# Kernel optimization log

Hardware: AMD Instinct MI355X
Metric: run time of the kernel (lower is better)

Reference implementation:

```python
import jax, jax.numpy as jnp
import numpy as np

B, C_IN, N, K, UP = 4, 128, 1024, 9, 4
EPS_BN = 1e-5


def _grid():
    # gen_grid(4): num_x=num_y=2, linspace(-0.2,0.2,2) -> (4,2)
    g = jnp.linspace(-0.2, 0.2, 2)
    x, y = jnp.meshgrid(g, g, indexing='ij')
    return jnp.stack([x, y], axis=-1).reshape(-1, 2)


def _knn(x, k, dilation):
    # x: (B,C,N). L2-normalize features, matrix pairwise dist, top-k, dilated select.
    nrm = jnp.sqrt(jnp.sum(x * x, axis=1, keepdims=True))
    xn = x / jnp.maximum(nrm, 1e-12)
    xt = xn.transpose(0, 2, 1)                      # (B,N,C)
    sq = jnp.sum(xt * xt, axis=-1)                  # (B,N)
    dist = sq[:, :, None] - 2.0 * jnp.einsum('bnc,bmc->bnm', xt, xt) + sq[:, None, :]
    _, idx = jax.lax.top_k(-dist, k * dilation)     # k*d nearest (incl. self)
    return idx[:, :, ::dilation]                    # (B,N,k)


def _bn(x, g, b, axes):
    # training-mode batchnorm over given axes, channel axis = 1
    m = jnp.mean(x, axis=axes, keepdims=True)
    v = jnp.mean((x - m) ** 2, axis=axes, keepdims=True)
    sh = [1] * x.ndim
    sh[1] = -1
    return (x - m) * jax.lax.rsqrt(v + EPS_BN) * g.reshape(sh) + b.reshape(sh)


def _edge_conv(x, k, dil, W, g, b):
    # DGCNN edge conv: gather neighbors, [x_i, x_j-x_i], 1x1 conv, BN, relu, max over k
    idx = _knn(x, k, dil)                                        # (B,N,k)
    x_j = jax.vmap(lambda xx, ii: xx[:, ii])(x, idx)             # (B,C,N,k)
    x_i = jnp.broadcast_to(x[..., None], x_j.shape)
    feat = jnp.concatenate([x_i, x_j - x_i], axis=1)             # (B,2C,N,k)
    out = jnp.einsum('oc,bcnk->bonk', W, feat)
    out = jax.nn.relu(_bn(out, g, b, (0, 2, 3)))
    return jnp.max(out, axis=-1)                                 # (B,Cout,N)


def _conv1d(x, W, b):
    return jnp.einsum('oc,bcn->bon', W, x) + b[None, :, None]


def _atten(x, Wf, bf, gf, bef, Wg, bg, gg, beg, Wh, bh, gh, beh, gamma):
    # attention_unit / RA_Layer1 math (C=130)
    f = jax.nn.relu(_bn(_conv1d(x, Wf, bf), gf, bef, (0, 2)))    # (B,C/4,M)
    g_ = jax.nn.relu(_bn(_conv1d(x, Wg, bg), gg, beg, (0, 2)))
    h = jax.nn.relu(_bn(_conv1d(x, Wh, bh), gh, beh, (0, 2)))    # (B,C,M)
    s = jnp.einsum('bcn,bcm->bnm', g_, f)                        # g^T @ f: (B,M,M)
    beta = jax.nn.softmax(s, axis=2)
    o = jnp.einsum('bcn,bnm->bcm', h, beta)                      # h @ beta
    return gamma * o + x


def _forward(inp, Wa, gna, bta, Wb, gnb, btb, Wf, bf, gf, bef, Wg, bg, gg, beg,
             Wh, bh, gh, beh, gamma, W1, b1, W2, b2):
    x1 = _edge_conv(inp, K, 1, Wa, gna, bta)                     # (B,256,N)
    x2 = _edge_conv(inp, K, 2, Wb, gnb, btb)                     # (B,256,N)
    x = jnp.concatenate([x1, x2], axis=1)                        # (B,512,N)
    net = x.transpose(0, 2, 1).reshape(B, N * UP, 128)           # (B,4N,128)
    grid = jnp.repeat(_grid(), N, axis=0)                        # (4N,2)
    grid = jnp.broadcast_to(grid[None], (B, N * UP, 2)).astype(net.dtype)
    net = jnp.concatenate([net, grid], axis=2).transpose(0, 2, 1)  # (B,130,4N)
    net = _atten(net, Wf, bf, gf, bef, Wg, bg, gg, beg, Wh, bh, gh, beh, gamma)
    net = jax.nn.relu(_conv1d(net, W1, b1))                      # 130->256
    net = jax.nn.relu(_conv1d(net, W2, b2))                      # 256->128
    return net                                                   # (B,128,4N)


def setup_inputs() -> dict:
    key = jax.random.key(0)
    ks = jax.random.split(key, 24)
    rn = lambda k, sh, s=0.05: jax.random.normal(k, sh, jnp.float32) * s
    d = {
        'inp': jax.random.normal(ks[0], (B, C_IN, N), jnp.float32),
        'Wa': rn(ks[1], (256, 256)), 'gna': 1.0 + rn(ks[2], (256,)), 'bta': rn(ks[3], (256,)),
        'Wb': rn(ks[4], (256, 256)), 'gnb': 1.0 + rn(ks[5], (256,)), 'btb': rn(ks[6], (256,)),
        'Wf': rn(ks[7], (32, 130)), 'bf': rn(ks[8], (32,)), 'gf': 1.0 + rn(ks[9], (32,)), 'bef': rn(ks[9], (32,)),
        'Wg': rn(ks[10], (32, 130)), 'bg': rn(ks[11], (32,)), 'gg': 1.0 + rn(ks[12], (32,)), 'beg': rn(ks[12], (32,)),
        'Wh': rn(ks[13], (130, 130)), 'bh': rn(ks[14], (130,)), 'gh': 1.0 + rn(ks[15], (130,)), 'beh': rn(ks[15], (130,)),
        'gamma': rn(ks[16], (), 1.0),
        'W1': rn(ks[17], (256, 130)), 'b1': rn(ks[18], (256,)),
        'W2': rn(ks[19], (128, 256)), 'b2': rn(ks[20], (128,)),
    }
    return d


def reference(inp, Wa, gna, bta, Wb, gnb, btb, Wf, bf, gf, bef, Wg, bg, gg, beg,
              Wh, bh, gh, beh, gamma, W1, b1, W2, b2):
    return _forward(inp, Wa, gna, bta, Wb, gnb, btb, Wf, bf, gf, bef, Wg, bg, gg, beg,
                    Wh, bh, gh, beh, gamma, W1, b1, W2, b2)
```

## Files before the change

### kernel.cpp

```cpp
#include <hip/hip_runtime.h>

namespace {
constexpr int NB = 4;
constexpr int CI = 128;
constexpr int NP = 1024;
constexpr int MM = 4096;
constexpr float EPSBN = 1e-5f;
constexpr float LOG2E = 1.4426950408889634f;

constexpr size_t OPS_SH = 2162688;
constexpr size_t OFF_OP   = 0;
constexpr size_t OFF_DIST = 0;
constexpr size_t OFF_PM   = 0;
constexpr size_t OFF_QM   = 2097152;
constexpr size_t OFF_HRAW = 0;
constexpr size_t OFF_FGRAW= 2359296;
constexpr size_t OFF_Y1   = 0;
constexpr size_t OFF_FGT  = 6488064;
constexpr size_t OFF_HB   = 7012352;
constexpr size_t OFF_A16  = 6488064;
constexpr size_t OFF_X16  = 8192000;
constexpr size_t OFF_LSE  = 9502720;
constexpr size_t OFF_LSEP = 9519104;
constexpr size_t OFF_STATS= 9650176;
constexpr size_t OFF_ABE  = 9715712;
constexpr size_t OFF_ABFG = 9716736;
constexpr size_t OFF_ABH  = 9716864;
constexpr size_t OFF_FGP  = 9717376;
constexpr size_t OFF_BIAS = 9725568;
constexpr size_t OFF_W16  = 9726208;
constexpr size_t OFF_KNN  = 9779712;
constexpr size_t OFF_XN   = 9853440;
constexpr size_t OFF_SQ   = 10377728;
constexpr size_t OFF_XR   = 10381824;
constexpr size_t OFF_WPQ  = 10643968;
constexpr size_t W16_FG = 0;
constexpr size_t W16_H  = 10240;
constexpr size_t W16_C1 = 33280;
constexpr size_t W16_C2 = 74240;
constexpr size_t B_FG = 0, B_H = 64, B_C1 = 208, B_C2 = 464;
}

typedef __attribute__((ext_vector_type(8))) short short8;
typedef __attribute__((ext_vector_type(4))) float f32x4;
#define MFMA16(A, B, C) __builtin_amdgcn_mfma_f32_16x16x32_bf16(A, B, C, 0, 0, 0)

__device__ inline unsigned short f2bf(float x) {
  unsigned int u = __float_as_uint(x);
  unsigned int r = u + 0x7fff + ((u >> 16) & 1);
  return (unsigned short)(r >> 16);
}
__device__ inline float bf2f(unsigned short s) {
  return __uint_as_float(((unsigned int)s) << 16);
}
__device__ inline unsigned cvtpk(float lo, float hi) {
  unsigned r;
  asm("v_cvt_pk_bf16_f32 %0, %1, %2" : "=v"(r) : "v"(lo), "v"(hi));
  return r;
}

__global__ __launch_bounds__(256) void k_prep(const float* __restrict__ Wf, const float* __restrict__ Wg,
                                              const float* __restrict__ Wh, const float* __restrict__ W1,
                                              const float* __restrict__ W2, const float* __restrict__ bf,
                                              const float* __restrict__ bg, const float* __restrict__ bh,
                                              const float* __restrict__ b1, const float* __restrict__ b2,
                                              const float* __restrict__ Wa, const float* __restrict__ Wb,
                                              unsigned short* __restrict__ W16, float* __restrict__ BIAS,
                                              unsigned short* __restrict__ WPQ) {
  int i = blockIdx.x * 256 + threadIdx.x;
  if (i < 107008) {
    float v = 0.f;
    if (i < 10240) { int o = i / 160, c = i % 160; if (c < 130) v = (o < 32) ? Wf[o * 130 + c] : Wg[(o - 32) * 130 + c]; }
    else if (i < 33280) { int r = i - 10240; int o = r / 160, c = r % 160; if (o < 130 && c < 130) v = Wh[o * 130 + c]; }
    else if (i < 74240) { int r = i - 33280; int o = r / 160, c = r % 160; if (c < 130) v = W1[o * 130 + c]; }
    else { int r = i - 74240; int o = r / 256, c = r % 256; v = W2[o * 256 + c]; }
    W16[i] = f2bf(v);
  } else if (i < 107648) {
    int j = i - 107008; float v = 0.f;
    if (j < 64) v = (j < 32) ? bf[j] : bg[j - 32];
    else if (j < 208) { int c = j - 64; if (c < 130) v = bh[c]; }
    else if (j < 464) v = b1[j - 208];
    else if (j < 592) v = b2[j - 464];
    BIAS[j] = v;
  } else if (i < 238720) {
    int j = i - 107648;
    int e = j >> 16;
    int rem = j & 65535;
    int pq = rem >> 15;
    int rr = rem & 32767;
    int o = rr >> 7, c = rr & 127;
    const float* W = e ? Wb : Wa;
    float w1 = W[o * 256 + c], w2 = W[o * 256 + 128 + c];
    float v = pq ? w2 : (w1 - w2);
    WPQ[j] = f2bf(v);
  }
}

__global__ __launch_bounds__(256) void k_norm(const float* __restrict__ x,
                                              float* __restrict__ xn,
                                              unsigned short* __restrict__ XR,
                                              float* __restrict__ sq) {
  int t = blockIdx.x * 256 + threadIdx.x;
  int b = t >> 10, n = t & 1023;
  const float* xb = x + (size_t)b * CI * NP + n;
  float ss = 0.f;
  #pragma unroll 4
  for (int c = 0; c < CI; ++c) { float v = xb[(size_t)c * NP]; ss += v * v; }
  float inv = 1.f / fmaxf(sqrtf(ss), 1e-12f);
  float* xo = xn + (size_t)b * CI * NP + n;
  float s2 = 0.f;
  for (int c0 = 0; c0 < 128; c0 += 8) {
    unsigned rw[4];
    #pragma unroll
    for (int j = 0; j < 4; ++j) {
      float va = xb[(size_t)(c0 + 2 * j) * NP];
      float vb = xb[(size_t)(c0 + 2 * j + 1) * NP];
      float na = va * inv, nb = vb * inv;
      s2 += na * na + nb * nb;
      xo[(size_t)(c0 + 2 * j) * NP] = na;
      xo[(size_t)(c0 + 2 * j + 1) * NP] = nb;
      rw[j] = (unsigned)f2bf(va) | ((unsigned)f2bf(vb) << 16);
    }
    uint4 r4 = {rw[0], rw[1], rw[2], rw[3]};
    *(uint4*)&XR[(size_t)t * 128 + c0] = r4;
  }
  sq[t] = s2;
}

__global__ __launch_bounds__(256) void k_dist(const float* __restrict__ xn,
                                              const float* __restrict__ sq,
                                              float* __restrict__ dist) {
  __shared__ float As[32][132], Bs[32][132];
  int t = threadIdx.x;
  int m0 = blockIdx.x * 128, n0 = blockIdx.y * 128, b = blockIdx.z;
  int mg = t & 15, ng = t >> 4;
  float acc[8][8];
  #pragma unroll
  for (int i = 0; i < 8; ++i)
    #pragma unroll
    for (int j = 0; j < 8; ++j) acc[i][j] = 0.f;
  for (int cc = 0; cc < 128; cc += 32) {
    __syncthreads();
    for (int idx = t; idx < 4096; idx += 256) {
      int c = idx >> 7, j = idx & 127;
      As[c][j] = xn[((size_t)b * CI + cc + c) * NP + n0 + j];
      Bs[c][j] = xn[((size_t)b * CI + cc + c) * NP + m0 + j];
    }
    __syncthreads();
    #pragma unroll
    for (int c = 0; c < 32; ++c) {
      float4 a0 = *(const float4*)&As[c][ng * 8];
      float4 a1 = *(const float4*)&As[c][ng * 8 + 4];
      float4 b0 = *(const float4*)&Bs[c][mg * 8];
      float4 b1 = *(const float4*)&Bs[c][mg * 8 + 4];
      float av[8] = {a0.x, a0.y, a0.z, a0.w, a1.x, a1.y, a1.z, a1.w};
      float bv[8] = {b0.x, b0.y, b0.z, b0.w, b1.x, b1.y, b1.z, b1.w};
      #pragma unroll
      for (int i = 0; i < 8; ++i)
        #pragma unroll
        for (int j = 0; j < 8; ++j) acc[i][j] += av[i] * bv[j];
    }
  }
  #pragma unroll
  for (int i = 0; i < 8; ++i) {
    int n = n0 + ng * 8 + i;
    float sn = sq[b * NP + n];
    #pragma unroll
    for (int jq = 0; jq < 2; ++jq) {
      float4 r;
      int mb = m0 + mg * 8 + jq * 4;
      r.x = sn + sq[b * NP + mb + 0] - 2.f * acc[i][jq * 4 + 0];
      r.y = sn + sq[b * NP + mb + 1] - 2.f * acc[i][jq * 4 + 1];
      r.z = sn + sq[b * NP + mb + 2] - 2.f * acc[i][jq * 4 + 2];
      r.w = sn + sq[b * NP + mb + 3] - 2.f * acc[i][jq * 4 + 3];
      *(float4*)&dist[((size_t)b * NP + n) * NP + mb] = r;
    }
  }
}

__global__ __launch_bounds__(64) void k_knn(const float* __restrict__ dist,
                                            int* __restrict__ knn) {
  int row = blockIdx.x;
  int l = threadIdx.x;
  const float* dr = dist + (size_t)row * NP;
  float d[16];
  #pragma unroll
  for (int i = 0; i < 16; ++i) d[i] = dr[l + 64 * i];
  for (int s = 0; s < 18; ++s) {
    float best = __builtin_inff(); int bslot = -1;
    #pragma unroll
    for (int i = 0; i < 16; ++i) if (d[i] < best) { best = d[i]; bslot = i; }
    int bidx = (bslot >= 0) ? (l + 64 * bslot) : 0x7fffffff;
    float bd = best; int bi = bidx;
    #pragma unroll
    for (int off = 32; off > 0; off >>= 1) {
      float od = __shfl_xor(bd, off);
      int   oi = __shfl_xor(bi, off);
      if (od < bd || (od == bd && oi < bi)) { bd = od; bi = oi; }
    }
    if (l == 0) knn[row * 18 + s] = bi;
    if ((bi & 63) == l) d[bi >> 6] = __builtin_inff();
  }
}

__global__ __launch_bounds__(256) void k_pqm(const unsigned short* __restrict__ XR,
                                             const unsigned short* __restrict__ WPQ,
                                             float* __restrict__ Pm,
                                             float* __restrict__ Qm) {
  int t = threadIdx.x; int w = t >> 6; int l = t & 63;
  int lm = l & 15, g = l >> 4;
  int nt = blockIdx.x, oq = blockIdx.y, z = blockIdx.z;
  int e = z >> 2, b = z & 3;
  int srow = nt * 64 + w * 16 + lm;
  const unsigned short* sp = XR + ((size_t)b * 1024 + srow) * 128 + 8 * g;
  const unsigned short* wpp = WPQ + ((size_t)(e * 2 + 0) * 256 + oq * 64 + lm) * 128 + 8 * g;
  const unsigned short* wqq = WPQ + ((size_t)(e * 2 + 1) * 256 + oq * 64 + lm) * 128 + 8 * g;
  f32x4 accp[4], accq[4];
  #pragma unroll
  for (int i = 0; i < 4; ++i) { accp[i] = {0.f, 0.f, 0.f, 0.f}; accq[i] = {0.f, 0.f, 0.f, 0.f}; }
  #pragma unroll
  for (int cc = 0; cc < 4; ++cc) {
    short8 bfr = *(const short8*)(sp + cc * 32);
    #pragma unroll
    for (int ct = 0; ct < 4; ++ct) {
      short8 ap = *(const short8*)(wpp + (size_t)ct * 16 * 128 + cc * 32);
      accp[ct] = MFMA16(ap, bfr, accp[ct]);
      short8 aq = *(const short8*)(wqq + (size_t)ct * 16 * 128 + cc * 32);
      accq[ct] = MFMA16(aq, bfr, accq[ct]);
    }
  }
  int eb = e * 4 + b;
  #pragma unroll
  for (int ct = 0; ct < 4; ++ct) {
    int o0 = oq * 64 + ct * 16 + 4 * g;
    float4 rp = {accp[ct][0], accp[ct][1], accp[ct][2], accp[ct][3]};
    float4 rq = {accq[ct][0], accq[ct][1], accq[ct][2], accq[ct][3]};
    *(float4*)&Pm[((size_t)eb * 1024 + srow) * 256 + o0] = rp;
    *(float4*)&Qm[((size_t)eb * 1024 + srow) * 256 + o0] = rq;
  }
}

__global__ __launch_bounds__(256) void k_edge_stats(const float* __restrict__ Pm,
                                                    const float* __restrict__ Qm,
                                                    const int* __restrict__ knn,
                                                    float* __restrict__ stats) {
  int o = threadIdx.x;
  int chunk = blockIdx.x, b = blockIdx.y, e = blockIdx.z;
  int eb = e * 4 + b;
  float s = 0.f, s2 = 0.f;
  for (int nn = 0; nn < 64; ++nn) {
    int n = chunk * 64 + nn;
    float p = Pm[((size_t)eb * 1024 + n) * 256 + o];
    const int* kn = knn + (b * 1024 + n) * 18;
    #pragma unroll
    for (int kk = 0; kk < 9; ++kk) {
      int j = kn[e ? 2 * kk : kk];
      float v = p + Qm[((size_t)eb * 1024 + j) * 256 + o];
      s += v; s2 += v * v;
    }
  }
  size_t idx = ((((size_t)e * 4 + b) * 16 + chunk) * 256 + o) * 2;
  stats[idx] = s; stats[idx + 1] = s2;
}

__global__ __launch_bounds__(256) void k_edge_fin(const float* __restrict__ stats,
                                                  const float* __restrict__ gna, const float* __restrict__ bta,
                                                  const float* __restrict__ gnb, const float* __restrict__ btb,
                                                  float* __restrict__ ab) {
  int i = blockIdx.x * 256 + threadIdx.x;
  if (i >= 512) return;
  int e = i >> 8, o = i & 255;
  float s = 0.f, s2 = 0.f;
  for (int b = 0; b < 4; ++b)
    for (int ch = 0; ch < 16; ++ch) {
      size_t idx = ((((size_t)e * 4 + b) * 16 + ch) * 256 + o) * 2;
      s += stats[idx]; s2 += stats[idx + 1];
    }
  float cnt = 4.0f * 1024.0f * 9.0f;
  float mean = s / cnt;
  float var = s2 / cnt - mean * mean;
  float g = e ? gnb[o] : gna[o];
  float bt = e ? btb[o] : bta[o];
  float alpha = g * rsqrtf(var + EPSBN);
  ab[i * 2] = alpha; ab[i * 2 + 1] = bt - mean * alpha;
}

__global__ __launch_bounds__(256) void k_edge_apply(const float* __restrict__ Pm,
                                                    const float* __restrict__ Qm,
                                                    const int* __restrict__ knn,
                                                    const float* __restrict__ ab,
                                                    unsigned short* __restrict__ X16) {
  __shared__ int knl[18];
  int t = threadIdx.x;
  int n = blockIdx.x, b = blockIdx.y;
  if (t < 18) knl[t] = knn[(b * 1024 + n) * 18 + t];
  __syncthreads();
  int e = t >> 7, oo = t & 127;
  int eb = e * 4 + b;
  const float* Pr = Pm + ((size_t)eb * 1024 + n) * 256;
  const float* Qb = Qm + (size_t)eb * 1024 * 256;
  float p0 = Pr[oo], p1 = Pr[oo + 128];
  float a0 = ab[(e * 256 + oo) * 2], be0 = ab[(e * 256 + oo) * 2 + 1];
  float a1 = ab[(e * 256 + oo + 128) * 2], be1 = ab[(e * 256 + oo + 128) * 2 + 1];
  float mx0 = -__builtin_inff(), mx1 = -__builtin_inff();
  #pragma unroll
  for (int kk = 0; kk < 9; ++kk) {
    int j = knl[e ? 2 * kk : kk];
    const float* Qr = Qb + (size_t)j * 256;
    mx0 = fmaxf(mx0, fmaf(a0, p0 + Qr[oo], be0));
    mx1 = fmaxf(mx1, fmaf(a1, p1 + Qr[oo + 128], be1));
  }
  int u0 = e << 1, u1 = (e << 1) | 1;
  X16[((size_t)b * MM + 4 * n + u0) * 160 + oo] = f2bf(fmaxf(mx0, 0.f));
  X16[((size_t)b * MM + 4 * n + u1) * 160 + oo] = f2bf(fmaxf(mx1, 0.f));
  if (t < 128) {
    int u = t >> 5, c = 128 + (t & 31);
    int gr = n >> 8;
    float v = (c == 128) ? ((gr < 2) ? -0.2f : 0.2f) : (c == 129) ? ((gr & 1) ? 0.2f : -0.2f) : 0.f;
    X16[((size_t)b * MM + 4 * n + u) * 160 + c] = f2bf(v);
  }
}

template <int KSTEPS, int CTPER, int OUTMODE, bool RELU>
__global__ __launch_bounds__(256) void k_convm(const unsigned short* __restrict__ src,
                                               const unsigned short* __restrict__ W16,
                                               const float* __restrict__ bias,
                                               float* __restrict__ dstF,
                                               unsigned short* __restrict__ dstB,
                                               int outld, int rows) {
  constexpr int LD = KSTEPS * 32;
  int t = threadIdx.x; int w = t >> 6; int l = t & 63;
  int lm = l & 15, g = l >> 4;
  int b = blockIdx.z; int ct0 = blockIdx.y * CTPER;
  int srow = blockIdx.x * 64 + w * 16 + lm;
  const unsigned short* sp = src + ((size_t)b * MM + srow) * LD + 8 * g;
  const unsigned short* wp = W16 + ((size_t)ct0 * 16 + lm) * LD + 8 * g;
  f32x4 acc[CTPER];
  #pragma unroll
  for (int i = 0; i < CTPER; ++i) acc[i] = {0.f, 0.f, 0.f, 0.f};
  #pragma unroll
  for (int cc = 0; cc < KSTEPS; ++cc) {
    short8 bfr = *(const short8*)(sp + cc * 32);
    #pragma unroll
    for (int ct = 0; ct < CTPER; ++ct) {
      short8 af = *(const short8*)(wp + (size_t)ct * 16 * LD + cc * 32);
      acc[ct] = MFMA16(af, bfr, acc[ct]);
    }
  }
  #pragma unroll
  for (int ct = 0; ct < CTPER; ++ct) {
    int o0 = (ct0 + ct) * 16 + 4 * g;
    float4 bv = *(const float4*)&bias[o0];
    float v[4] = {acc[ct][0] + bv.x, acc[ct][1] + bv.y, acc[ct][2] + bv.z, acc[ct][3] + bv.w};
    if (RELU) { v[0] = fmaxf(v[0], 0.f); v[1] = fmaxf(v[1], 0.f); v[2] = fmaxf(v[2], 0.f); v[3] = fmaxf(v[3], 0.f); }
    if (OUTMODE == 0) {
      float4 r = {v[0], v[1], v[2], v[3]};
      *(float4*)&dstF[((size_t)b * MM + srow) * outld + o0] = r;
    } else if (OUTMODE == 1) {
      uint2 pk;
      pk.x = cvtpk(v[0], v[1]);
      pk.y = cvtpk(v[2], v[3]);
      *(uint2*)&dstB[((size_t)b * MM + srow) * outld + o0] = pk;
    } else {
      #pragma unroll
      for (int r = 0; r < 4; ++r)
        dstF[((size_t)b * rows + o0 + r) * MM + srow] = v[r];
    }
  }
}

__global__ __launch_bounds__(256) void k_fgstats(const float* __restrict__ FGraw,
                                                 float* __restrict__ FGP) {
  __shared__ float red[4][64][2];
  int t = threadIdx.x; int c = t & 63, rq = t >> 6;
  int blk = blockIdx.x;
  float s = 0.f, s2 = 0.f;
  for (int k = 0; k < 64; ++k) {
    int r = blk * 256 + rq + 4 * k;
    float v = FGraw[(size_t)r * 64 + c];
    s += v; s2 += v * v;
  }
  red[rq][c][0] = s; red[rq][c][1] = s2;
  __syncthreads();
  if (t < 64) {
    float a = 0.f, a2 = 0.f;
    #pragma unroll
    for (int q = 0; q < 4; ++q) { a += red[q][t][0]; a2 += red[q][t][1]; }
    FGP[((size_t)blk * 64 + t) * 2] = a; FGP[((size_t)blk * 64 + t) * 2 + 1] = a2;
  }
}

__global__ __launch_bounds__(64) void k_fgfin(const float* __restrict__ FGP,
                                              const float* __restrict__ gf, const float* __restrict__ bef,
                                              const float* __restrict__ gg, const float* __restrict__ beg,
                                              float* __restrict__ ab) {
  int c = threadIdx.x;
  float s = 0.f, s2 = 0.f;
  for (int blk = 0; blk < 64; ++blk) { s += FGP[((size_t)blk * 64 + c) * 2]; s2 += FGP[((size_t)blk * 64 + c) * 2 + 1]; }
  float cnt = 16384.f;
  float mean = s / cnt, var = s2 / cnt - mean * mean;
  float gv = (c < 32) ? gf[c] : gg[c - 32];
  float bv = (c < 32) ? bef[c] : beg[c - 32];
  float alpha = gv * rsqrtf(var + EPSBN);
  ab[c * 2] = alpha; ab[c * 2 + 1] = bv - mean * alpha;
}

__global__ __launch_bounds__(256) void k_bnstats(const float* __restrict__ src,
                                                 const float* __restrict__ g,
                                                 const float* __restrict__ be,
                                                 float* __restrict__ ab, int ldC) {
  int o = blockIdx.x;
  int t = threadIdx.x;
  float s = 0.f, s2 = 0.f;
  for (int b = 0; b < NB; ++b) {
    const float* r = src + ((size_t)b * ldC + o) * MM;
    for (int m = t; m < MM; m += 256) { float v = r[m]; s += v; s2 += v * v; }
  }
  __shared__ float rs[256], rs2[256];
  rs[t] = s; rs2[t] = s2;
  __syncthreads();
  for (int off = 128; off > 0; off >>= 1) {
    if (t < off) { rs[t] += rs[t + off]; rs2[t] += rs2[t + off]; }
    __syncthreads();
  }
  if (t == 0) {
    float cnt = 16384.0f;
    float mean = rs[0] / cnt, var = rs2[0] / cnt - mean * mean;
    float alpha = g[o] * rsqrtf(var + EPSBN);
    ab[o * 2] = alpha; ab[o * 2 + 1] = be[o] - mean * alpha;
  }
}

__global__ __launch_bounds__(256) void k_cvtFG(const float* __restrict__ FGraw,
                                               const float* __restrict__ ab,
                                               unsigned short* __restrict__ FGT) {
  int i = blockIdx.x * 256 + threadIdx.x;
  int row = i >> 3, c0 = (i & 7) * 8;
  float sc = (c0 < 32) ? LOG2E : 1.0f;
  float vv[8];
  float4 u0 = *(const float4*)&FGraw[(size_t)row * 64 + c0];
  float4 u1 = *(const float4*)&FGraw[(size_t)row * 64 + c0 + 4];
  vv[0] = u0.x; vv[1] = u0.y; vv[2] = u0.z; vv[3] = u0.w;
  vv[4] = u1.x; vv[5] = u1.y; vv[6] = u1.z; vv[7] = u1.w;
  uint4 pk;
  unsigned pw[4];
  #pragma unroll
  for (int h = 0; h < 4; ++h) {
    int c = c0 + 2 * h;
    float a0 = ab[c * 2] * sc, b0 = ab[c * 2 + 1] * sc;
    float a1 = ab[(c + 1) * 2] * sc, b1 = ab[(c + 1) * 2 + 1] * sc;
    float x0 = fmaxf(fmaf(a0, vv[2 * h], b0), 0.f);
    float x1 = fmaxf(fmaf(a1, vv[2 * h + 1], b1), 0.f);
    pw[h] = cvtpk(x0, x1);
  }
  pk.x = pw[0]; pk.y = pw[1]; pk.z = pw[2]; pk.w = pw[3];
  *(uint4*)&FGT[(size_t)row * 64 + c0] = pk;
}

__global__ __launch_bounds__(256) void k_cvtH(const float* __restrict__ src,
                                              const float* __restrict__ ab,
                                              unsigned short* __restrict__ dst) {
  int i = blockIdx.x * 256 + threadIdx.x;
  int m4 = i & 1023; int c = (i >> 10) % 144; int b = i / (144 * 1024);
  ushort4 ov = {0, 0, 0, 0};
  if (c < 130) {
    float4 v = *(const float4*)&src[((size_t)b * 144 + c) * MM + m4 * 4];
    float a = ab[c * 2], be = ab[c * 2 + 1];
    ov.x = f2bf(fmaxf(fmaf(a, v.x, be), 0.f));
    ov.y = f2bf(fmaxf(fmaf(a, v.y, be), 0.f));
    ov.z = f2bf(fmaxf(fmaf(a, v.z, be), 0.f));
    ov.w = f2bf(fmaxf(fmaf(a, v.w, be), 0.f));
  }
  *(ushort4*)&dst[((size_t)b * 144 + c) * MM + m4 * 4] = ov;
}

__global__ __launch_bounds__(256) void k_zlse(const unsigned short* __restrict__ FGT,
                                              float* __restrict__ LSEP) {
  int t = threadIdx.x; int w = t >> 6; int l = t & 63;
  int b = blockIdx.z; int ms = blockIdx.y;
  int n0 = blockIdx.x * 64 + w * 16;
  int lm = l & 15, g = l >> 4;
  f32x4 z4 = {0.f, 0.f, 0.f, 0.f};
  short8 af = *(const short8*)&FGT[((size_t)b * MM + n0 + lm) * 64 + 32 + 8 * g];
  float rm[4], zz[4];
  #pragma unroll
  for (int r = 0; r < 4; ++r) { rm[r] = -__builtin_inff(); zz[r] = 0.f; }
  for (int it = 0; it < 16; ++it) {
    int m0 = ms * 1024 + it * 64;
    short8 bfr[4];
    #pragma unroll
    for (int mi = 0; mi < 4; ++mi)
      bfr[mi] = *(const short8*)&FGT[((size_t)b * MM + m0 + mi * 16 + lm) * 64 + 8 * g];
    f32x4 d[4];
    #pragma unroll
    for (int mi = 0; mi < 4; ++mi) d[mi] = MFMA16(af, bfr[mi], z4);
    #pragma unroll
    for (int r = 0; r < 4; ++r) {
      float tm = fmaxf(fmaxf(d[0][r], d[1][r]), fmaxf(d[2][r], d[3][r]));
      float nm = fmaxf(rm[r], tm);
      zz[r] = zz[r] * exp2f(rm[r] - nm)
            + exp2f(d[0][r] - nm) + exp2f(d[1][r] - nm)
            + exp2f(d[2][r] - nm) + exp2f(d[3][r] - nm);
      rm[r] = nm;
    }
  }
  #pragma unroll
  for (int off = 1; off < 16; off <<= 1) {
    #pragma unroll
    for (int r = 0; r < 4; ++r) {
      float om = __shfl_xor(rm[r], off);
      float oz = __shfl_xor(zz[r], off);
      float nm = fmaxf(rm[r], om);
      zz[r] = zz[r] * exp2f(rm[r] - nm) + oz * exp2f(om - nm);
      rm[r] = nm;
    }
  }
  if (lm == 0) {
    #pragma unroll
    for (int r = 0; r < 4; ++r) {
      int n = n0 + 4 * g + r;
      size_t idx = ((size_t)ms * 16384 + (size_t)b * MM + n) * 2;
      LSEP[idx] = rm[r]; LSEP[idx + 1] = zz[r];
    }
  }
}

__global__ __launch_bounds__(256) void k_lsered(const float* __restrict__ LSEP,
                                                float* __restrict__ LSE) {
  int bn = blockIdx.x * 256 + threadIdx.x;
  float rm = -__builtin_inff(), zz = 0.f;
  #pragma unroll
  for (int ms = 0; ms < 4; ++ms) {
    float m = LSEP[((size_t)ms * 16384 + bn) * 2];
    float z = LSEP[((size_t)ms * 16384 + bn) * 2 + 1];
    float nm = fmaxf(rm, m);
    zz = zz * exp2f(rm - nm) + z * exp2f(m - nm);
    rm = nm;
  }
  LSE[bn] = rm + log2f(zz);
}

__global__ __launch_bounds__(256) void k_omfma(const unsigned short* __restrict__ FGT,
                                               const unsigned short* __restrict__ HB,
                                               const float* __restrict__ LSE,
                                               unsigned short* __restrict__ Opart) {
  __shared__ __align__(16) unsigned short Hs[2][144 * 40];
  int t = threadIdx.x; int w = t >> 6; int l = t & 63;
  int b = blockIdx.y; int split = blockIdx.z;
  int lm = l & 15, g = l >> 4;
  int mcol0 = blockIdx.x * 128 + w * 32 + lm;
  int mcol1 = mcol0 + 16;
  f32x4 z4 = {0.f, 0.f, 0.f, 0.f};
  short8 Ff0 = *(const short8*)&FGT[((size_t)b * MM + mcol0) * 64 + 8 * g];
  short8 Ff1 = *(const short8*)&FGT[((size_t)b * MM + mcol1) * 64 + 8 * g];
  f32x4 acc0[9], acc1[9];
  #pragma unroll
  for (int ct = 0; ct < 9; ++ct) { acc0[ct] = z4; acc1[ct] = z4; }
  const int nchunks = (split < 2) ? 22 : 21;
  const int startc = split * 21 + ((split < 2) ? split : 2);
  const int start = startc * 32;
  const unsigned short* gptr = FGT + ((size_t)b * MM + lm) * 64 + 32 + 8 * g;
  const unsigned short* hsrc = HB + (size_t)b * 144 * MM;
  const float* lbase = LSE + (size_t)b * MM + 4 * g;
  int src01 = lm + 16 * (2 * (g & 1));
  int src23 = src01 + 16;
  bool hi = g >= 2;
  int sidx0 = t, sidx1 = t + 256, sidx2 = t + 512;
  int ch0 = sidx0 >> 2, sg0 = sidx0 & 3;
  int ch1 = sidx1 >> 2, sg1 = sidx1 & 3;
  int ch2 = (sidx2 < 576) ? (sidx2 >> 2) : 0;
  int sg2 = sidx2 & 3;
  bool has2 = sidx2 < 576;

  {
    uint4 r0 = *(const uint4*)(hsrc + (size_t)ch0 * MM + start + sg0 * 8);
    uint4 r1 = *(const uint4*)(hsrc + (size_t)ch1 * MM + start + sg1 * 8);
    uint4 r2 = has2 ? *(const uint4*)(hsrc + (size_t)ch2 * MM + start + sg2 * 8) : uint4{0,0,0,0};
    *(uint4*)&Hs[0][ch0 * 40 + sg0 * 8] = r0;
    *(uint4*)&Hs[0][ch1 * 40 + sg1 * 8] = r1;
    if (has2) *(uint4*)&Hs[0][ch2 * 40 + sg2 * 8] = r2;
  }
  short8 a0 = *(const short8*)(gptr + (size_t)start * 64);
  short8 a1 = *(const short8*)(gptr + (size_t)(start + 16) * 64);
  float4 l0 = *(const float4*)(lbase + start);
  float4 l1 = *(const float4*)(lbase + start + 16);
  __syncthreads();

  for (int it = 0; it < nchunks; ++it) {
    int n0 = start + it * 32;
    int cur = it & 1;
    bool more = (it + 1 < nchunks);
    int n1 = more ? (n0 + 32) : start;
    uint4 r0, r1, r2;
    if (more) {
      r0 = *(const uint4*)(hsrc + (size_t)ch0 * MM + n1 + sg0 * 8);
      r1 = *(const uint4*)(hsrc + (size_t)ch1 * MM + n1 + sg1 * 8);
      if (has2) r2 = *(const uint4*)(hsrc + (size_t)ch2 * MM + n1 + sg2 * 8);
    }
    short8 na0 = *(const short8*)(gptr + (size_t)n1 * 64);
    short8 na1 = *(const short8*)(gptr + (size_t)(n1 + 16) * 64);
    float4 nl0 = *(const float4*)(lbase + n1);
    float4 nl1 = *(const float4*)(lbase + n1 + 16);
    short8 hf[9];
    #pragma unroll
    for (int ct = 0; ct < 9; ++ct)
      hf[ct] = *(const short8*)&Hs[cur][(lm + 16 * ct) * 40 + g * 8];
    f32x4 s00 = MFMA16(a0, Ff0, z4);
    f32x4 s10 = MFMA16(a1, Ff0, z4);
    f32x4 s01 = MFMA16(a0, Ff1, z4);
    f32x4 s11 = MFMA16(a1, Ff1, z4);
    float le0[4] = {l0.x, l0.y, l0.z, l0.w};
    float le1[4] = {l1.x, l1.y, l1.z, l1.w};
    unsigned pk00[2], pk10[2], pk01[2], pk11[2];
    #pragma unroll
    for (int h2 = 0; h2 < 2; ++h2) {
      pk00[h2] = cvtpk(exp2f(s00[2*h2] - le0[2*h2]), exp2f(s00[2*h2+1] - le0[2*h2+1]));
      pk10[h2] = cvtpk(exp2f(s10[2*h2] - le1[2*h2]), exp2f(s10[2*h2+1] - le1[2*h2+1]));
      pk01[h2] = cvtpk(exp2f(s01[2*h2] - le0[2*h2]), exp2f(s01[2*h2+1] - le0[2*h2+1]));
      pk11[h2] = cvtpk(exp2f(s11[2*h2] - le1[2*h2]), exp2f(s11[2*h2+1] - le1[2*h2+1]));
    }
    unsigned a0w = (unsigned)__shfl((int)pk00[0], src01);
    unsigned b0w = (unsigned)__shfl((int)pk10[0], src01);
    unsigned a1w = (unsigned)__shfl((int)pk00[1], src01);
    unsigned b1w = (unsigned)__shfl((int)pk10[1], src01);
    unsigned a2w = (unsigned)__shfl((int)pk00[0], src23);
    unsigned b2w = (unsigned)__shfl((int)pk10[0], src23);
    unsigned a3w = (unsigned)__shfl((int)pk00[1], src23);
    unsigned b3w = (unsigned)__shfl((int)pk10[1], src23);
    union { unsigned u[4]; short8 s; } bu0;
    bu0.u[0] = hi ? b0w : a0w; bu0.u[1] = hi ? b1w : a1w;
    bu0.u[2] = hi ? b2w : a2w; bu0.u[3] = hi ? b3w : a3w;
    short8 bfrag0 = bu0.s;
    unsigned c0w = (unsigned)__shfl((int)pk01[0], src01);
    unsigned d0w = (unsigned)__shfl((int)pk11[0], src01);
    unsigned c1w = (unsigned)__shfl((int)pk01[1], src01);
    unsigned d1w = (unsigned)__shfl((int)pk11[1], src01);
    unsigned c2w = (unsigned)__shfl((int)pk01[0], src23);
    unsigned d2w = (unsigned)__shfl((int)pk11[0], src23);
    unsigned c3w = (unsigned)__shfl((int)pk01[1], src23);
    unsigned d3w = (unsigned)__shfl((int)pk11[1], src23);
    union { unsigned u[4]; short8 s; } bu1;
    bu1.u[0] = hi ? d0w : c0w; bu1.u[1] = hi ? d1w : c1w;
    bu1.u[2] = hi ? d2w : c2w; bu1.u[3] = hi ? d3w : c3w;
    short8 bfrag1 = bu1.s;
    __builtin_amdgcn_s_setprio(1);
    #pragma unroll
    for (int ct = 0; ct < 9; ++ct) {
      acc0[ct] = MFMA16(hf[ct], bfrag0, acc0[ct]);
      acc1[ct] = MFMA16(hf[ct], bfrag1, acc1[ct]);
    }
    __builtin_amdgcn_s_setprio(0);
    if (more) {
      *(uint4*)&Hs[cur ^ 1][ch0 * 40 + sg0 * 8] = r0;
      *(uint4*)&Hs[cur ^ 1][ch1 * 40 + sg1 * 8] = r1;
      if (has2) *(uint4*)&Hs[cur ^ 1][ch2 * 40 + sg2 * 8] = r2;
    }
    a0 = na0; a1 = na1; l0 = nl0; l1 = nl1;
    __syncthreads();
  }

  unsigned short* op0 = Opart + (size_t)split * OPS_SH + ((size_t)b * MM + mcol0) * 132;
  unsigned short* op1 = Opart + (size_t)split * OPS_SH + ((size_t)b * MM + mcol1) * 132;
  #pragma unroll
  for (int ct = 0; ct < 9; ++ct) {
    int c0 = ct * 16 + 4 * g;
    if (c0 < 132) {
      uint2 p0, p1;
      p0.x = cvtpk(acc0[ct][0], acc0[ct][1]);
      p0.y = cvtpk(acc0[ct][2], acc0[ct][3]);
      p1.x = cvtpk(acc1[ct][0], acc1[ct][1]);
      p1.y = cvtpk(acc1[ct][2], acc1[ct][3]);
      *(uint2*)&op0[c0] = p0;
      *(uint2*)&op1[c0] = p1;
    }
  }
}

__global__ __launch_bounds__(256) void k_ored(const unsigned short* __restrict__ Op,
                                              const unsigned short* __restrict__ X16,
                                              const float* __restrict__ gma,
                                              unsigned short* __restrict__ A16) {
  int i = blockIdx.x * 256 + threadIdx.x;
  int row = i / 20, c8 = i % 20;
  int c0 = c8 * 8;
  unsigned short* ap = A16 + (size_t)row * 160 + c0;
  if (c0 >= 136) {
    uint4 z = {0, 0, 0, 0};
    *(uint4*)ap = z;
    return;
  }
  float gm = gma[0];
  float ov[8] = {0.f, 0.f, 0.f, 0.f, 0.f, 0.f, 0.f, 0.f};
  #pragma unroll
  for (int s = 0; s < 6; ++s) {
    const unsigned short* base = Op + (size_t)s * OPS_SH + (size_t)row * 132 + c0;
    uint2 u = *(const uint2*)base;
    ov[0] += bf2f((unsigned short)(u.x & 0xffff));
    ov[1] += bf2f((unsigned short)(u.x >> 16));
    ov[2] += bf2f((unsigned short)(u.y & 0xffff));
    ov[3] += bf2f((unsigned short)(u.y >> 16));
    if (c0 + 4 < 132) {
      uint2 v = *(const uint2*)(base + 4);
      ov[4] += bf2f((unsigned short)(v.x & 0xffff));
      ov[5] += bf2f((unsigned short)(v.x >> 16));
      ov[6] += bf2f((unsigned short)(v.y & 0xffff));
      ov[7] += bf2f((unsigned short)(v.y >> 16));
    }
  }
  short8 xv = *(const short8*)(X16 + (size_t)row * 160 + c0);
  unsigned pw[4];
  #pragma unroll
  for (int h = 0; h < 4; ++h) {
    int ca = c0 + 2 * h, cb = c0 + 2 * h + 1;
    float xa = bf2f((unsigned short)xv[2 * h]);
    float xb = bf2f((unsigned short)xv[2 * h + 1]);
    float va = (ca < 132) ? (gm * ov[2 * h] + xa) : 0.f;
    float vb = (cb < 132) ? (gm * ov[2 * h + 1] + xb) : 0.f;
    pw[h] = (unsigned)f2bf(va) | ((unsigned)f2bf(vb) << 16);
  }
  uint4 pk = {pw[0], pw[1], pw[2], pw[3]};
  *(uint4*)ap = pk;
}

extern "C" void kernel_launch(void* const* d_in, const int* in_sizes, int n_in,
                              void* d_out, int out_size, void* d_ws, size_t ws_size,
                              hipStream_t stream) {
  const float* inp = (const float*)d_in[0];
  const float* Wa  = (const float*)d_in[1];
  const float* gna = (const float*)d_in[2];
  const float* bta = (const float*)d_in[3];
  const float* Wb  = (const float*)d_in[4];
  const float* gnb = (const float*)d_in[5];
  const float* btb = (const float*)d_in[6];
  const float* Wf  = (const float*)d_in[7];
  const float* bf  = (const float*)d_in[8];
  const float* gf  = (const float*)d_in[9];
  const float* bef = (const float*)d_in[10];
  const float* Wg  = (const float*)d_in[11];
  const float* bg  = (const float*)d_in[12];
  const float* gg  = (const float*)d_in[13];
  const float* beg = (const float*)d_in[14];
  const float* Wh  = (const float*)d_in[15];
  const float* bh  = (const float*)d_in[16];
  const float* gh  = (const float*)d_in[17];
  const float* beh = (const float*)d_in[18];
  const float* gamma = (const float*)d_in[19];
  const float* W1  = (const float*)d_in[20];
  const float* b1  = (const float*)d_in[21];
  const float* W2  = (const float*)d_in[22];
  const float* b2  = (const float*)d_in[23];
  float* out = (float*)d_out;

  float* ws = (float*)d_ws;
  float* DIST = ws + OFF_DIST;
  float* PM   = ws + OFF_PM;
  float* QM   = ws + OFF_QM;
  float* HRAW = ws + OFF_HRAW;
  float* FGRAW= ws + OFF_FGRAW;
  unsigned short* OP16 = (unsigned short*)(ws + OFF_OP);
  unsigned short* FGT = (unsigned short*)(ws + OFF_FGT);
  unsigned short* HBB = (unsigned short*)(ws + OFF_HB);
  unsigned short* A16 = (unsigned short*)(ws + OFF_A16);
  unsigned short* X16 = (unsigned short*)(ws + OFF_X16);
  unsigned short* Y1  = (unsigned short*)(ws + OFF_Y1);
  float* LSEB = ws + OFF_LSE;
  float* LSEP = ws + OFF_LSEP;
  float* STATS= ws + OFF_STATS;
  float* ABE  = ws + OFF_ABE;
  float* ABFG = ws + OFF_ABFG;
  float* ABH  = ws + OFF_ABH;
  float* FGP  = ws + OFF_FGP;
  float* BIAS = ws + OFF_BIAS;
  unsigned short* W16 = (unsigned short*)(ws + OFF_W16);
  int*   KNNI = (int*)(ws + OFF_KNN);
  float* XN   = ws + OFF_XN;
  unsigned short* XR = (unsigned short*)(ws + OFF_XR);
  unsigned short* WPQ = (unsigned short*)(ws + OFF_WPQ);
  float* SQ   = ws + OFF_SQ;

  k_prep<<<933, 256, 0, stream>>>(Wf, Wg, Wh, W1, W2, bf, bg, bh, b1, b2, Wa, Wb, W16, BIAS, WPQ);
  k_norm<<<16, 256, 0, stream>>>(inp, XN, XR, SQ);
  k_dist<<<dim3(8, 8, 4), 256, 0, stream>>>(XN, SQ, DIST);
  k_knn<<<4096, 64, 0, stream>>>(DIST, KNNI);
  k_pqm<<<dim3(16, 4, 8), 256, 0, stream>>>(XR, WPQ, PM, QM);
  k_edge_stats<<<dim3(16, 4, 2), 256, 0, stream>>>(PM, QM, KNNI, STATS);
  k_edge_fin<<<2, 256, 0, stream>>>(STATS, gna, bta, gnb, btb, ABE);
  k_edge_apply<<<dim3(1024, 4), 256, 0, stream>>>(PM, QM, KNNI, ABE, X16);
  k_convm<5, 2, 0, false><<<dim3(64, 2, 4), 256, 0, stream>>>(X16, W16 + W16_FG, BIAS + B_FG, FGRAW, nullptr, 64, 0);
  k_convm<5, 3, 2, false><<<dim3(64, 3, 4), 256, 0, stream>>>(X16, W16 + W16_H, BIAS + B_H, HRAW, nullptr, 0, 144);
  k_fgstats<<<64, 256, 0, stream>>>(FGRAW, FGP);
  k_fgfin<<<1, 64, 0, stream>>>(FGP, gf, bef, gg, beg, ABFG);
  k_bnstats<<<130, 256, 0, stream>>>(HRAW, gh, beh, ABH, 144);
  k_cvtFG<<<512, 256, 0, stream>>>(FGRAW, ABFG, FGT);
  k_cvtH<<<2304, 256, 0, stream>>>(HRAW, ABH, HBB);
  k_zlse<<<dim3(64, 4, 4), 256, 0, stream>>>(FGT, LSEP);
  k_lsered<<<64, 256, 0, stream>>>(LSEP, LSEB);
  k_omfma<<<dim3(32, 4, 6), 256, 0, stream>>>(FGT, HBB, LSEB, OP16);
  k_ored<<<1280, 256, 0, stream>>>(OP16, X16, gamma, A16);
  k_convm<5, 8, 1, true><<<dim3(64, 2, 4), 256, 0, stream>>>(A16, W16 + W16_C1, BIAS + B_C1, nullptr, Y1, 256, 0);
  k_convm<8, 4, 2, true><<<dim3(64, 2, 4), 256, 0, stream>>>(Y1, W16 + W16_C2, BIAS + B_C2, out, nullptr, 0, 128);
}
```

Baseline: 317.3 us.

## Merge prep and norm kernels, fold fgfin into cvtFG, shrink dist tile

Combines the weight-prep and normalization kernels into one launch by block range, and folds the single-block FG batchnorm finalize into each k_cvtFG block, which recomputes the alpha/beta in shared memory. The pairwise-distance kernel tile is narrowed from 128x128 to 128x64 so it launches twice as many blocks. Together these cut two kernel launches and their serialization gaps and raise dist-kernel parallelism. In exchange, every cvtFG block redundantly reduces the FG partial stats, and the smaller dist tile lowers per-thread arithmetic reuse.

After: 313.2 us. About the same (-1.3%).

```diff
diff --git a/kernel.cpp b/kernel.cpp
--- a/kernel.cpp
+++ b/kernel.cpp
@@ -59,91 +59,95 @@
   return r;
 }
 
-__global__ __launch_bounds__(256) void k_prep(const float* __restrict__ Wf, const float* __restrict__ Wg,
+__global__ __launch_bounds__(256) void k_init(const float* __restrict__ Wf, const float* __restrict__ Wg,
                                               const float* __restrict__ Wh, const float* __restrict__ W1,
                                               const float* __restrict__ W2, const float* __restrict__ bf,
                                               const float* __restrict__ bg, const float* __restrict__ bh,
                                               const float* __restrict__ b1, const float* __restrict__ b2,
                                               const float* __restrict__ Wa, const float* __restrict__ Wb,
                                               unsigned short* __restrict__ W16, float* __restrict__ BIAS,
-                                              unsigned short* __restrict__ WPQ) {
-  int i = blockIdx.x * 256 + threadIdx.x;
-  if (i < 107008) {
-    float v = 0.f;
-    if (i < 10240) { int o = i / 160, c = i % 160; if (c < 130) v = (o < 32) ? Wf[o * 130 + c] : Wg[(o - 32) * 130 + c]; }
-    else if (i < 33280) { int r = i - 10240; int o = r / 160, c = r % 160; if (o < 130 && c < 130) v = Wh[o * 130 + c]; }
-    else if (i < 74240) { int r = i - 33280; int o = r / 160, c = r % 160; if (c < 130) v = W1[o * 130 + c]; }
-    else { int r = i - 74240; int o = r / 256, c = r % 256; v = W2[o * 256 + c]; }
-    W16[i] = f2bf(v);
-  } else if (i < 107648) {
-    int j = i - 107008; float v = 0.f;
-    if (j < 64) v = (j < 32) ? bf[j] : bg[j - 32];
-    else if (j < 208) { int c = j - 64; if (c < 130) v = bh[c]; }
-    else if (j < 464) v = b1[j - 208];
-    else if (j < 592) v = b2[j - 464];
-    BIAS[j] = v;
-  } else if (i < 238720) {
-    int j = i - 107648;
-    int e = j >> 16;
-    int rem = j & 65535;
-    int pq = rem >> 15;
-    int rr = rem & 32767;
-    int o = rr >> 7, c = rr & 127;
-    const float* W = e ? Wb : Wa;
-    float w1 = W[o * 256 + c], w2 = W[o * 256 + 128 + c];
-    float v = pq ? w2 : (w1 - w2);
-    WPQ[j] = f2bf(v);
-  }
-}
-
-__global__ __launch_bounds__(256) void k_norm(const float* __restrict__ x,
+                                              unsigned short* __restrict__ WPQ,
+                                              const float* __restrict__ x,
                                               float* __restrict__ xn,
                                               unsigned short* __restrict__ XR,
                                               float* __restrict__ sq) {
-  int t = blockIdx.x * 256 + threadIdx.x;
-  int b = t >> 10, n = t & 1023;
-  const float* xb = x + (size_t)b * CI * NP + n;
-  float ss = 0.f;
-  #pragma unroll 4
-  for (int c = 0; c < CI; ++c) { float v = xb[(size_t)c * NP]; ss += v * v; }
-  float inv = 1.f / fmaxf(sqrtf(ss), 1e-12f);
-  float* xo = xn + (size_t)b * CI * NP + n;
-  float s2 = 0.f;
-  for (int c0 = 0; c0 < 128; c0 += 8) {
-    unsigned rw[4];
-    #pragma unroll
-    for (int j = 0; j < 4; ++j) {
-      float va = xb[(size_t)(c0 + 2 * j) * NP];
-      float vb = xb[(size_t)(c0 + 2 * j + 1) * NP];
-      float na = va * inv, nb = vb * inv;
-      s2 += na * na + nb * nb;
-      xo[(size_t)(c0 + 2 * j) * NP] = na;
-      xo[(size_t)(c0 + 2 * j + 1) * NP] = nb;
-      rw[j] = (unsigned)f2bf(va) | ((unsigned)f2bf(vb) << 16);
-    }
-    uint4 r4 = {rw[0], rw[1], rw[2], rw[3]};
-    *(uint4*)&XR[(size_t)t * 128 + c0] = r4;
-  }
-  sq[t] = s2;
+  if (blockIdx.x < 933) {
+    int i = blockIdx.x * 256 + threadIdx.x;
+    if (i < 107008) {
+      float v = 0.f;
+      if (i < 10240) { int o = i / 160, c = i % 160; if (c < 130) v = (o < 32) ? Wf[o * 130 + c] : Wg[(o - 32) * 130 + c]; }
+      else if (i < 33280) { int r = i - 10240; int o = r / 160, c = r % 160; if (o < 130 && c < 130) v = Wh[o * 130 + c]; }
+      else if (i < 74240) { int r = i - 33280; int o = r / 160, c = r % 160; if (c < 130) v = W1[o * 130 + c]; }
+      else { int r = i - 74240; int o = r / 256, c = r % 256; v = W2[o * 256 + c]; }
+      W16[i] = f2bf(v);
+    } else if (i < 107648) {
+      int j = i - 107008; float v = 0.f;
+      if (j < 64) v = (j < 32) ? bf[j] : bg[j - 32];
+      else if (j < 208) { int c = j - 64; if (c < 130) v = bh[c]; }
+      else if (j < 464) v = b1[j - 208];
+      else if (j < 592) v = b2[j - 464];
+      BIAS[j] = v;
+    } else if (i < 238720) {
+      int j = i - 107648;
+      int e = j >> 16;
+      int rem = j & 65535;
+      int pq = rem >> 15;
+      int rr = rem & 32767;
+      int o = rr >> 7, c = rr & 127;
+      const float* W = e ? Wb : Wa;
+      float w1 = W[o * 256 + c], w2 = W[o * 256 + 128 + c];
+      float v = pq ? w2 : (w1 - w2);
+      WPQ[j] = f2bf(v);
+    }
+  } else {
+    int t = (blockIdx.x - 933) * 256 + threadIdx.x;
+    int b = t >> 10, n = t & 1023;
+    const float* xb = x + (size_t)b * CI * NP + n;
+    float ss = 0.f;
+    #pragma unroll 4
+    for (int c = 0; c < CI; ++c) { float v = xb[(size_t)c * NP]; ss += v * v; }
+    float inv = 1.f / fmaxf(sqrtf(ss), 1e-12f);
+    float* xo = xn + (size_t)b * CI * NP + n;
+    float s2 = 0.f;
+    for (int c0 = 0; c0 < 128; c0 += 8) {
+      unsigned rw[4];
+      #pragma unroll
+      for (int j = 0; j < 4; ++j) {
+        float va = xb[(size_t)(c0 + 2 * j) * NP];
+        float vb = xb[(size_t)(c0 + 2 * j + 1) * NP];
+        float na = va * inv, nb = vb * inv;
+        s2 += na * na + nb * nb;
+        xo[(size_t)(c0 + 2 * j) * NP] = na;
+        xo[(size_t)(c0 + 2 * j + 1) * NP] = nb;
+        rw[j] = (unsigned)f2bf(va) | ((unsigned)f2bf(vb) << 16);
+      }
+      uint4 r4 = {rw[0], rw[1], rw[2], rw[3]};
+      *(uint4*)&XR[(size_t)t * 128 + c0] = r4;
+    }
+    sq[t] = s2;
+  }
 }
 
 __global__ __launch_bounds__(256) void k_dist(const float* __restrict__ xn,
                                               const float* __restrict__ sq,
                                               float* __restrict__ dist) {
-  __shared__ float As[32][132], Bs[32][132];
+  __shared__ float As[32][132], Bs[32][68];
   int t = threadIdx.x;
-  int m0 = blockIdx.x * 128, n0 = blockIdx.y * 128, b = blockIdx.z;
+  int m0 = blockIdx.x * 64, n0 = blockIdx.y * 128, b = blockIdx.z;
   int mg = t & 15, ng = t >> 4;
-  float acc[8][8];
+  float acc[8][4];
   #pragma unroll
   for (int i = 0; i < 8; ++i)
     #pragma unroll
-    for (int j = 0; j < 8; ++j) acc[i][j] = 0.f;
+    for (int j = 0; j < 4; ++j) acc[i][j] = 0.f;
   for (int cc = 0; cc < 128; cc += 32) {
     __syncthreads();
     for (int idx = t; idx < 4096; idx += 256) {
       int c = idx >> 7, j = idx & 127;
       As[c][j] = xn[((size_t)b * CI + cc + c) * NP + n0 + j];
+    }
+    for (int idx = t; idx < 2048; idx += 256) {
+      int c = idx >> 6, j = idx & 63;
       Bs[c][j] = xn[((size_t)b * CI + cc + c) * NP + m0 + j];
     }
     __syncthreads();
@@ -151,30 +155,26 @@
     for (int c = 0; c < 32; ++c) {
       float4 a0 = *(const float4*)&As[c][ng * 8];
       float4 a1 = *(const float4*)&As[c][ng * 8 + 4];
-      float4 b0 = *(const float4*)&Bs[c][mg * 8];
-      float4 b1 = *(const float4*)&Bs[c][mg * 8 + 4];
+      float4 b0 = *(const float4*)&Bs[c][mg * 4];
       float av[8] = {a0.x, a0.y, a0.z, a0.w, a1.x, a1.y, a1.z, a1.w};
-      float bv[8] = {b0.x, b0.y, b0.z, b0.w, b1.x, b1.y, b1.z, b1.w};
+      float bv[4] = {b0.x, b0.y, b0.z, b0.w};
       #pragma unroll
       for (int i = 0; i < 8; ++i)
         #pragma unroll
-        for (int j = 0; j < 8; ++j) acc[i][j] += av[i] * bv[j];
+        for (int j = 0; j < 4; ++j) acc[i][j] += av[i] * bv[j];
     }
   }
   #pragma unroll
   for (int i = 0; i < 8; ++i) {
     int n = n0 + ng * 8 + i;
     float sn = sq[b * NP + n];
-    #pragma unroll
-    for (int jq = 0; jq < 2; ++jq) {
-      float4 r;
-      int mb = m0 + mg * 8 + jq * 4;
-      r.x = sn + sq[b * NP + mb + 0] - 2.f * acc[i][jq * 4 + 0];
-      r.y = sn + sq[b * NP + mb + 1] - 2.f * acc[i][jq * 4 + 1];
-      r.z = sn + sq[b * NP + mb + 2] - 2.f * acc[i][jq * 4 + 2];
-      r.w = sn + sq[b * NP + mb + 3] - 2.f * acc[i][jq * 4 + 3];
-      *(float4*)&dist[((size_t)b * NP + n) * NP + mb] = r;
-    }
+    int mb = m0 + mg * 4;
+    float4 r;
+    r.x = sn + sq[b * NP + mb + 0] - 2.f * acc[i][0];
+    r.y = sn + sq[b * NP + mb + 1] - 2.f * acc[i][1];
+    r.z = sn + sq[b * NP + mb + 2] - 2.f * acc[i][2];
+    r.w = sn + sq[b * NP + mb + 3] - 2.f * acc[i][3];
+    *(float4*)&dist[((size_t)b * NP + n) * NP + mb] = r;
   }
 }
 
@@ -390,21 +390,6 @@
   }
 }
 
-__global__ __launch_bounds__(64) void k_fgfin(const float* __restrict__ FGP,
-                                              const float* __restrict__ gf, const float* __restrict__ bef,
-                                              const float* __restrict__ gg, const float* __restrict__ beg,
-                                              float* __restrict__ ab) {
-  int c = threadIdx.x;
-  float s = 0.f, s2 = 0.f;
-  for (int blk = 0; blk < 64; ++blk) { s += FGP[((size_t)blk * 64 + c) * 2]; s2 += FGP[((size_t)blk * 64 + c) * 2 + 1]; }
-  float cnt = 16384.f;
-  float mean = s / cnt, var = s2 / cnt - mean * mean;
-  float gv = (c < 32) ? gf[c] : gg[c - 32];
-  float bv = (c < 32) ? bef[c] : beg[c - 32];
-  float alpha = gv * rsqrtf(var + EPSBN);
-  ab[c * 2] = alpha; ab[c * 2 + 1] = bv - mean * alpha;
-}
-
 __global__ __launch_bounds__(256) void k_bnstats(const float* __restrict__ src,
                                                  const float* __restrict__ g,
                                                  const float* __restrict__ be,
@@ -432,9 +417,27 @@
 }
 
 __global__ __launch_bounds__(256) void k_cvtFG(const float* __restrict__ FGraw,
-                                               const float* __restrict__ ab,
+                                               const float* __restrict__ FGP,
+                                               const float* __restrict__ gf, const float* __restrict__ bef,
+                                               const float* __restrict__ gg, const float* __restrict__ beg,
                                                unsigned short* __restrict__ FGT) {
-  int i = blockIdx.x * 256 + threadIdx.x;
+  __shared__ float sab[128];
+  int t = threadIdx.x;
+  if (t < 64) {
+    float s = 0.f, s2 = 0.f;
+    for (int blk = 0; blk < 64; ++blk) {
+      s += FGP[((size_t)blk * 64 + t) * 2];
+      s2 += FGP[((size_t)blk * 64 + t) * 2 + 1];
+    }
+    float cnt = 16384.f;
+    float mean = s / cnt, var = s2 / cnt - mean * mean;
+    float gv = (t < 32) ? gf[t] : gg[t - 32];
+    float bv = (t < 32) ? bef[t] : beg[t - 32];
+    float alpha = gv * rsqrtf(var + EPSBN);
+    sab[t * 2] = alpha; sab[t * 2 + 1] = bv - mean * alpha;
+  }
+  __syncthreads();
+  int i = blockIdx.x * 256 + t;
   int row = i >> 3, c0 = (i & 7) * 8;
   float sc = (c0 < 32) ? LOG2E : 1.0f;
   float vv[8];
@@ -447,8 +450,8 @@
   #pragma unroll
   for (int h = 0; h < 4; ++h) {
     int c = c0 + 2 * h;
-    float a0 = ab[c * 2] * sc, b0 = ab[c * 2 + 1] * sc;
-    float a1 = ab[(c + 1) * 2] * sc, b1 = ab[(c + 1) * 2 + 1] * sc;
+    float a0 = sab[c * 2] * sc, b0 = sab[c * 2 + 1] * sc;
+    float a1 = sab[(c + 1) * 2] * sc, b1 = sab[(c + 1) * 2 + 1] * sc;
     float x0 = fmaxf(fmaf(a0, vv[2 * h], b0), 0.f);
     float x1 = fmaxf(fmaf(a1, vv[2 * h + 1], b1), 0.f);
     pw[h] = cvtpk(x0, x1);
@@ -767,7 +770,6 @@
   float* LSEP = ws + OFF_LSEP;
   float* STATS= ws + OFF_STATS;
   float* ABE  = ws + OFF_ABE;
-  float* ABFG = ws + OFF_ABFG;
   float* ABH  = ws + OFF_ABH;
   float* FGP  = ws + OFF_FGP;
   float* BIAS = ws + OFF_BIAS;
@@ -778,9 +780,9 @@
   unsigned short* WPQ = (unsigned short*)(ws + OFF_WPQ);
   float* SQ   = ws + OFF_SQ;
 
-  k_prep<<<933, 256, 0, stream>>>(Wf, Wg, Wh, W1, W2, bf, bg, bh, b1, b2, Wa, Wb, W16, BIAS, WPQ);
-  k_norm<<<16, 256, 0, stream>>>(inp, XN, XR, SQ);
-  k_dist<<<dim3(8, 8, 4), 256, 0, stream>>>(XN, SQ, DIST);
+  k_init<<<949, 256, 0, stream>>>(Wf, Wg, Wh, W1, W2, bf, bg, bh, b1, b2, Wa, Wb, W16, BIAS, WPQ,
+                                  inp, XN, XR, SQ);
+  k_dist<<<dim3(16, 8, 4), 256, 0, stream>>>(XN, SQ, DIST);
   k_knn<<<4096, 64, 0, stream>>>(DIST, KNNI);
   k_pqm<<<dim3(16, 4, 8), 256, 0, stream>>>(XR, WPQ, PM, QM);
   k_edge_stats<<<dim3(16, 4, 2), 256, 0, stream>>>(PM, QM, KNNI, STATS);
@@ -789,9 +791,8 @@
   k_convm<5, 2, 0, false><<<dim3(64, 2, 4), 256, 0, stream>>>(X16, W16 + W16_FG, BIAS + B_FG, FGRAW, nullptr, 64, 0);
   k_convm<5, 3, 2, false><<<dim3(64, 3, 4), 256, 0, stream>>>(X16, W16 + W16_H, BIAS + B_H, HRAW, nullptr, 0, 144);
   k_fgstats<<<64, 256, 0, stream>>>(FGRAW, FGP);
-  k_fgfin<<<1, 64, 0, stream>>>(FGP, gf, bef, gg, beg, ABFG);
   k_bnstats<<<130, 256, 0, stream>>>(HRAW, gh, beh, ABH, 144);
-  k_cvtFG<<<512, 256, 0, stream>>>(FGRAW, ABFG, FGT);
+  k_cvtFG<<<512, 256, 0, stream>>>(FGRAW, FGP, gf, bef, gg, beg, FGT);
   k_cvtH<<<2304, 256, 0, stream>>>(HRAW, ABH, HBB);
   k_zlse<<<dim3(64, 4, 4), 256, 0, stream>>>(FGT, LSEP);
   k_lsered<<<64, 256, 0, stream>>>(LSEP, LSEB);
```
